# Performance work log

Measured on AMD Instinct MI355X. Metric: run time of the kernel, lower is better.

Reference implementation:

```python
import jax, jax.numpy as jnp
import numpy as np

N_NODES = 50000
N_EDGES = 800000
N_REL = 8
OUT_CH = 64      # latent dim of z
HID = 128        # hidden_channels
IN_CH = 128      # reconstructed feature dim
NEG_SLOPE = 0.2


def rgat_conv(x, src, dst, edge_type, weight, q, k, bias, num_nodes):
    """PyG RGATConv, heads=1, dim=1, additive-self-attention, across-relation.
    x: [N, in]; weight: [R, in, out]; q,k: [out, 1]; bias: [out]."""
    # per-relation transform of all nodes, then per-edge gather (same math as
    # per-edge bmm with weight[edge_type], avoids [E, in, out] intermediate)
    x_all = jnp.einsum('ni,rio->nro', x, weight)          # [N, R, out]
    x_j = x_all[src, edge_type]                            # [E, out]
    x_i = x_all[dst, edge_type]                            # [E, out]
    alpha = (x_i @ q + x_j @ k)[:, 0]                      # [E]
    alpha = jax.nn.leaky_relu(alpha, NEG_SLOPE)
    # scatter-softmax over destination neighborhoods
    m = jax.ops.segment_max(alpha, dst, num_segments=num_nodes)
    m = jnp.where(jnp.isfinite(m), m, 0.0)                 # empty segments -> 0
    ex = jnp.exp(alpha - m[dst])
    denom = jax.ops.segment_sum(ex, dst, num_segments=num_nodes)
    a = ex / (denom[dst] + 1e-16)                          # [E]
    out = jax.ops.segment_sum(a[:, None] * x_j, dst, num_segments=num_nodes)
    return out + bias


def setup_inputs() -> dict:
    key = jax.random.key(0)
    ks = jax.random.split(key, 12)
    z = jax.random.normal(ks[0], (N_NODES, OUT_CH), dtype=jnp.float32)
    edge_index = jax.random.randint(ks[1], (2, N_EDGES), 0, N_NODES, dtype=jnp.int32)
    edge_type = jax.random.randint(ks[2], (N_EDGES,), 0, N_REL, dtype=jnp.int32)

    def glorot(k_, shape):
        fan = shape[-2] + shape[-1]
        return jax.random.normal(k_, shape, dtype=jnp.float32) * jnp.sqrt(2.0 / fan)

    return {
        'z': z,
        'lin_w': glorot(ks[3], (HID, OUT_CH)),
        'lin_b': jnp.zeros((HID,), dtype=jnp.float32),
        'w1': glorot(ks[4], (N_REL, HID, HID)),
        'q1': glorot(ks[5], (HID, 1)),
        'k1': glorot(ks[6], (HID, 1)),
        'b1': jnp.zeros((HID,), dtype=jnp.float32),
        'w2': glorot(ks[7], (N_REL, HID, IN_CH)),
        'q2': glorot(ks[8], (IN_CH, 1)),
        'k2': glorot(ks[9], (IN_CH, 1)),
        'b2': jnp.zeros((IN_CH,), dtype=jnp.float32),
        'edge_index': edge_index,
        'edge_type': edge_type,
    }


def reference(z, lin_w, lin_b, w1, q1, k1, b1, w2, q2, k2, b2, edge_index, edge_type):
    num_nodes = z.shape[0]
    src, dst = edge_index[0], edge_index[1]
    h = z @ lin_w.T + lin_b                                 # nn.Linear
    h = jax.nn.relu(rgat_conv(h, src, dst, edge_type, w1, q1, k1, b1, num_nodes))
    # dropout is identity in eval mode
    recon_x = rgat_conv(h, src, dst, edge_type, w2, q2, k2, b2, num_nodes)
    return recon_x
```

## Files before the change

### kernel.cpp

```cpp
#include <hip/hip_runtime.h>
#include <hip/hip_bf16.h>
#include <cstdint>
#include <cstddef>

#define N_NODES 50000
#define N_EDGES 800000
#define NSEG    (N_NODES * 8)
#define HIST_BLKS 3125
#define WPREP_BLKS 1040
#define GLIN_BLKS 782
#define QK_BLKS 196

using frag_t = __attribute__((ext_vector_type(8))) short;
using f32x4  = __attribute__((ext_vector_type(4))) float;

typedef const __attribute__((address_space(1))) void* gptr_t;
typedef __attribute__((address_space(3))) void* lptr_t;

__device__ __forceinline__ short f2bf(float x) {
    __hip_bfloat16 h = __float2bfloat16(x);
    return *reinterpret_cast<short*>(&h);
}
__device__ __forceinline__ float bf2f(unsigned int u) {
    union { unsigned int i; float f; } v;
    v.i = u << 16;
    return v.f;
}
__device__ __forceinline__ float bf2f_hi(unsigned int u) {
    union { unsigned int i; float f; } v;
    v.i = u & 0xFFFF0000u;
    return v.f;
}
__device__ __forceinline__ unsigned int packbf2(float lo, float hi) {
    unsigned int a = (unsigned short)f2bf(lo);
    unsigned int b = (unsigned short)f2bf(hi);
    return a | (b << 16);
}


__global__ __launch_bounds__(256) void prep_mega(
        const int* __restrict__ dst, const int* __restrict__ et,
        int* __restrict__ deg8,
        const float* __restrict__ W1, const float* __restrict__ q1v,
        const float* __restrict__ k1v,
        const float* __restrict__ W2, const float* __restrict__ q2v,
        const float* __restrict__ k2v,
        short* __restrict__ Bf1, short* __restrict__ Bf2,
        float* __restrict__ wq1, float* __restrict__ wk1,
        float* __restrict__ wq2, float* __restrict__ wk2,
        const float* __restrict__ z, const float* __restrict__ lin_w,
        const float* __restrict__ lin_b,
        unsigned short* __restrict__ hb) {
    __shared__ float smem[32 * 64 + 32 * 128];
    int b = blockIdx.x, t = threadIdx.x;

    if (b < HIST_BLKS) {
        int e = b * 256 + t;
        if (e < N_EDGES) atomicAdd(&deg8[dst[e] * 8 + et[e]], 1);
        return;
    }
    b -= HIST_BLKS;

    if (b < WPREP_BLKS) {
        int g0 = b * 256 + t;
        int layer = (g0 >= 133120) ? 1 : 0;
        int g = g0 - layer * 133120;
        const float* W  = layer ? W2  : W1;
        const float* qv = layer ? q2v : q1v;
        const float* kv = layer ? k2v : k1v;
        short* Bf = layer ? Bf2 : Bf1;
        float* wq = layer ? wq2 : wq1;
        float* wk = layer ? wk2 : wk1;
        if (g < 131072) {
            int kk = g >> 7, o = g & 127;
            float v = W[(size_t)kk * 128 + o];
            Bf[(((size_t)(kk >> 3) * 128) + o) * 8 + (kk & 7)] = f2bf(v);
        } else {
            int h = g - 131072;
            if (h < 2048) {
                int which = h >> 10;
                int r = (h >> 7) & 7;
                int i = h & 127;
                const float* vec = which ? kv : qv;
                const float* wrow = W + ((size_t)r * 128 + i) * 128;
                float acc = 0.f;
                #pragma unroll 4
                for (int o = 0; o < 128; o++) acc = fmaf(wrow[o], vec[o], acc);
                (which ? wk : wq)[r * 128 + i] = acc;
            }
        }
        return;
    }
    b -= WPREP_BLKS;

    {
        float (*As)[64]  = (float (*)[64])smem;
        float (*Bs)[128] = (float (*)[128])(smem + 32 * 64);
        const int Kdim = 64;
        int n0 = b * 64;
        int rg = t >> 4, cg = t & 15;
        int an = t >> 2, ak = (t & 3) * 8;
        float acc[4][8] = {};

        for (int k0 = 0; k0 < Kdim; k0 += 32) {
            int gn = n0 + an;
            if (gn < N_NODES) {
                const float* ap = z + (size_t)gn * Kdim + k0 + ak;
                float4 v0 = *(const float4*)ap;
                float4 v1 = *(const float4*)(ap + 4);
                As[ak + 0][an] = v0.x; As[ak + 1][an] = v0.y;
                As[ak + 2][an] = v0.z; As[ak + 3][an] = v0.w;
                As[ak + 4][an] = v1.x; As[ak + 5][an] = v1.y;
                As[ak + 6][an] = v1.z; As[ak + 7][an] = v1.w;
            } else {
                #pragma unroll
                for (int c = 0; c < 8; c++) As[ak + c][an] = 0.f;
            }
            {
                int o = t >> 1, kh = (t & 1) * 16;
                const float* bp = lin_w + (size_t)o * Kdim + k0 + kh;
                #pragma unroll
                for (int j = 0; j < 4; j++) {
                    float4 v = ((const float4*)bp)[j];
                    Bs[kh + j * 4 + 0][o] = v.x;
                    Bs[kh + j * 4 + 1][o] = v.y;
                    Bs[kh + j * 4 + 2][o] = v.z;
                    Bs[kh + j * 4 + 3][o] = v.w;
                }
            }
            __syncthreads();
            #pragma unroll
            for (int k = 0; k < 32; k++) {
                float a[4], bb[8];
                *(float4*)&a[0] = *(const float4*)&As[k][rg * 4];
                *(float4*)&bb[0] = *(const float4*)&Bs[k][cg * 8];
                *(float4*)&bb[4] = *(const float4*)&Bs[k][cg * 8 + 4];
                #pragma unroll
                for (int i = 0; i < 4; i++)
                    #pragma unroll
                    for (int j = 0; j < 8; j++)
                        acc[i][j] = fmaf(a[i], bb[j], acc[i][j]);
            }
            __syncthreads();
        }
        #pragma unroll
        for (int i = 0; i < 4; i++) {
            int gn = n0 + rg * 4 + i;
            if (gn < N_NODES) {
                unsigned short us[8];
                #pragma unroll
                for (int j = 0; j < 8; j++)
                    us[j] = (unsigned short)f2bf(acc[i][j] + lin_b[cg * 8 + j]);
                *(int4*)(hb + (size_t)gn * 128 + cg * 8) = *(int4*)&us[0];
            }
        }
    }
}


__global__ __launch_bounds__(256) void scan_part(const int* __restrict__ deg8,
                                                 int* __restrict__ part, int M) {
    __shared__ int red[256];
    int t = threadIdx.x;
    int idx = blockIdx.x * 1024 + t * 4;
    int s = 0;
    if (idx + 3 < M) {
        int4 d = *(const int4*)(deg8 + idx);
        s = d.x + d.y + d.z + d.w;
    } else {
        for (int c = 0; c < 4; c++) if (idx + c < M) s += deg8[idx + c];
    }
    red[t] = s;
    __syncthreads();
    #pragma unroll
    for (int off = 128; off; off >>= 1) {
        if (t < off) red[t] += red[t + off];
        __syncthreads();
    }
    if (t == 0) part[blockIdx.x] = red[0];
}

__global__ __launch_bounds__(512) void scan_mid(int* __restrict__ part, int nparts,
                                                int* __restrict__ rowp, int M) {
    __shared__ int buf[512];
    int t = threadIdx.x;
    int own = (t < nparts) ? part[t] : 0;
    buf[t] = own;
    __syncthreads();
    for (int off = 1; off < 512; off <<= 1) {
        int v = buf[t];
        int u = (t >= off) ? buf[t - off] : 0;
        __syncthreads();
        buf[t] = v + u;
        __syncthreads();
    }
    if (t < nparts) part[t] = buf[t] - own;
    if (t == 511) rowp[M] = buf[511];
}

__global__ __launch_bounds__(256) void scan_fix(const int* __restrict__ deg8,
                                                const int* __restrict__ part,
                                                int* __restrict__ rowp,
                                                int* __restrict__ cursor, int M) {
    __shared__ int wsum[4];
    int t = threadIdx.x, lane = t & 63, w = t >> 6;
    int idx = blockIdx.x * 1024 + t * 4;
    int v0 = 0, v1 = 0, v2 = 0, v3 = 0;
    if (idx + 3 < M) {
        int4 d = *(const int4*)(deg8 + idx);
        v0 = d.x; v1 = d.y; v2 = d.z; v3 = d.w;
    } else {
        if (idx     < M) v0 = deg8[idx];
        if (idx + 1 < M) v1 = deg8[idx + 1];
        if (idx + 2 < M) v2 = deg8[idx + 2];
        if (idx + 3 < M) v3 = deg8[idx + 3];
    }
    int tsum = v0 + v1 + v2 + v3;
    int sc = tsum;
    #pragma unroll
    for (int off = 1; off < 64; off <<= 1) {
        int u = __shfl_up(sc, off, 64);
        if (lane >= off) sc += u;
    }
    if (lane == 63) wsum[w] = sc;
    __syncthreads();
    int woff = 0;
    for (int i = 0; i < w; i++) woff += wsum[i];
    int excl = part[blockIdx.x] + woff + sc - tsum;
    if (idx     < M) { rowp[idx]     = excl; cursor[idx]     = excl; } excl += v0;
    if (idx + 1 < M) { rowp[idx + 1] = excl; cursor[idx + 1] = excl; } excl += v1;
    if (idx + 2 < M) { rowp[idx + 2] = excl; cursor[idx + 2] = excl; } excl += v2;
    if (idx + 3 < M) { rowp[idx + 3] = excl; cursor[idx + 3] = excl; }
}


__global__ __launch_bounds__(256) void fill_qk(
        const int* __restrict__ src, const int* __restrict__ dst,
        const int* __restrict__ et, int* __restrict__ cursor,
        int* __restrict__ sorted,
        const unsigned short* __restrict__ xb,
        const float* __restrict__ wq, const float* __restrict__ wk,
        float* __restrict__ Q, float* __restrict__ K) {
    int b = blockIdx.x, t = threadIdx.x;

    if (b < HIST_BLKS) {
        int e = b * 256 + t;
        if (e < N_EDGES) {
            int pos = atomicAdd(&cursor[dst[e] * 8 + et[e]], 1);
            sorted[pos] = src[e] | (et[e] << 16);
        }
        return;
    }
    b -= HIST_BLKS;

    int n = b * 256 + t;
    if (n >= N_NODES) return;
    const uint2* row = (const uint2*)(xb + (size_t)n * 128);
    float aq[8] = {}, ak[8] = {};
    for (int i = 0; i < 32; i++) {
        uint2 d = row[i];
        float x0 = bf2f(d.x & 0xFFFFu);
        float x1 = bf2f(d.x >> 16);
        float x2 = bf2f(d.y & 0xFFFFu);
        float x3 = bf2f(d.y >> 16);
        int c = i * 4;
        #pragma unroll
        for (int r = 0; r < 8; r++) {
            const float* wqr = wq + r * 128 + c;
            const float* wkr = wk + r * 128 + c;
            aq[r] = fmaf(x0, wqr[0], fmaf(x1, wqr[1], fmaf(x2, wqr[2], fmaf(x3, wqr[3], aq[r]))));
            ak[r] = fmaf(x0, wkr[0], fmaf(x1, wkr[1], fmaf(x2, wkr[2], fmaf(x3, wkr[3], ak[r]))));
        }
    }
    float4* qp = (float4*)(Q + (size_t)n * 8);
    qp[0] = *(float4*)&aq[0];
    qp[1] = *(float4*)&aq[4];
    float4* kp = (float4*)(K + (size_t)n * 8);
    kp[0] = *(float4*)&ak[0];
    kp[1] = *(float4*)&ak[4];
}


__global__ __launch_bounds__(256) void qk_table_kernel(const unsigned short* __restrict__ xb,
                                                       const float* __restrict__ wq,
                                                       const float* __restrict__ wk,
                                                       float* __restrict__ Q,
                                                       float* __restrict__ K, int N) {
    int n = blockIdx.x * 256 + threadIdx.x;
    if (n >= N) return;
    const uint2* row = (const uint2*)(xb + (size_t)n * 128);
    float aq[8] = {}, ak[8] = {};
    for (int i = 0; i < 32; i++) {
        uint2 d = row[i];
        float x0 = bf2f(d.x & 0xFFFFu);
        float x1 = bf2f(d.x >> 16);
        float x2 = bf2f(d.y & 0xFFFFu);
        float x3 = bf2f(d.y >> 16);
        int c = i * 4;
        #pragma unroll
        for (int r = 0; r < 8; r++) {
            const float* wqr = wq + r * 128 + c;
            const float* wkr = wk + r * 128 + c;
            aq[r] = fmaf(x0, wqr[0], fmaf(x1, wqr[1], fmaf(x2, wqr[2], fmaf(x3, wqr[3], aq[r]))));
            ak[r] = fmaf(x0, wkr[0], fmaf(x1, wkr[1], fmaf(x2, wkr[2], fmaf(x3, wkr[3], ak[r]))));
        }
    }
    float4* qp = (float4*)(Q + (size_t)n * 8);
    qp[0] = *(float4*)&aq[0];
    qp[1] = *(float4*)&aq[4];
    float4* kp = (float4*)(K + (size_t)n * 8);
    kp[0] = *(float4*)&ak[0];
    kp[1] = *(float4*)&ak[4];
}


__global__ __launch_bounds__(512, 8) void fused_agg_gemm(
        const unsigned short* __restrict__ hb,
        const float* __restrict__ Q,
        const float* __restrict__ Kt,
        const int* __restrict__ rowp8,
        const int* __restrict__ sorted,
        const short* __restrict__ Bf,
        const float* __restrict__ bias,
        float* __restrict__ Cout,
        unsigned short* __restrict__ hbout,
        int N, int relu) {
    __shared__ short s_tile[16 * 1024];
    __shared__ uint2 stash[8][64];
    __shared__ int wcnt;
    unsigned int* sdw = (unsigned int*)s_tile;
    const char* hbB = (const char*)hb;

    int t = threadIdx.x;
    int w = t >> 6, lane = t & 63;
    int lhi = lane >> 4, llo = lane & 15;
    unsigned int lv4 = (unsigned int)lane * 4u;
    int n0 = blockIdx.x * 16;

    if (t == 0) wcnt = 0;
    __syncthreads();

    for (;;) {
        int row;
        if (lane == 0) row = atomicAdd(&wcnt, 1);
        row = __shfl(row, 0, 64);
        if (row >= 16) break;
        int n = n0 + row;
        float2 acc = {0.f, 0.f};
        int rcur = 0;
        auto flushw = [&](unsigned int val) {
            int kb = rcur * 16 + (lane >> 2);
            sdw[kb * 64 + ((row ^ (kb & 15)) * 4) + (lane & 3)] = val;
        };
        if (n >= N) {
            while (rcur < 8) { flushw(0u); rcur++; }
            continue;
        }
        int beg = rowp8[n * 8];
        int end = rowp8[n * 8 + 8];
        int deg = end - beg;
        if (deg == 0) {
            while (rcur < 8) { flushw(0u); rcur++; }
            continue;
        }

        if (deg <= 64) {
            int pk = 0;
            float a = -INFINITY;
            if (lane < deg) {
                pk = sorted[beg + lane];
                int srcn = pk & 0xFFFF, etj = pk >> 16;
                a = Q[(size_t)n * 8 + etj] + Kt[(size_t)srcn * 8 + etj];
                a = (a > 0.f) ? a : 0.2f * a;
            }
            float m = a;
            #pragma unroll
            for (int off = 32; off; off >>= 1) m = fmaxf(m, __shfl_xor(m, off, 64));
            float e = (lane < deg) ? __expf(a - m) : 0.f;
            float sum = e;
            #pragma unroll
            for (int off = 32; off; off >>= 1) sum += __shfl_xor(sum, off, 64);
            float wgt = e / (sum + 1e-16f);
            stash[w][lane] = make_uint2((unsigned int)(pk & 0xFFFF) << 8,
                                        (__float_as_uint(wgt) & ~7u) | (unsigned int)(pk >> 16));

            int j = 0;
            for (; j + 8 <= deg; j += 8) {
                uint2 ee[8]; unsigned int dd[8];
                #pragma unroll
                for (int i = 0; i < 8; i++) ee[i] = stash[w][j + i];
                #pragma unroll
                for (int i = 0; i < 8; i++)
                    dd[i] = *(const unsigned int*)(hbB + (ee[i].x | lv4));
                #pragma unroll
                for (int i = 0; i < 8; i++) {
                    int e0 = (int)(ee[i].y & 7u);
                    float w0 = __uint_as_float(ee[i].y);
                    while (rcur < e0) { flushw(packbf2(acc.x, acc.y)); acc.x = acc.y = 0.f; rcur++; }
                    acc.x = fmaf(w0, bf2f(dd[i]),    acc.x);
                    acc.y = fmaf(w0, bf2f_hi(dd[i]), acc.y);
                }
            }
            for (; j < deg; j++) {
                uint2 e1 = stash[w][j];
                unsigned int d0 = *(const unsigned int*)(hbB + (e1.x | lv4));
                int e0 = (int)(e1.y & 7u);
                float w0 = __uint_as_float(e1.y);
                while (rcur < e0) { flushw(packbf2(acc.x, acc.y)); acc.x = acc.y = 0.f; rcur++; }
                acc.x = fmaf(w0, bf2f(d0),    acc.x);
                acc.y = fmaf(w0, bf2f_hi(d0), acc.y);
            }
            while (rcur < 8) { flushw(packbf2(acc.x, acc.y)); acc.x = acc.y = 0.f; rcur++; }
        } else {
            auto logit = [&](int j) -> float {
                int pk2 = sorted[beg + j];
                int srcn = pk2 & 0xFFFF, etj = pk2 >> 16;
                float aa = Q[(size_t)n * 8 + etj] + Kt[(size_t)srcn * 8 + etj];
                return (aa > 0.f) ? aa : 0.2f * aa;
            };
            float m = -INFINITY;
            for (int j = lane; j < deg; j += 64) m = fmaxf(m, logit(j));
            #pragma unroll
            for (int off = 32; off; off >>= 1) m = fmaxf(m, __shfl_xor(m, off, 64));
            float sum = 0.f;
            for (int j = lane; j < deg; j += 64) sum += __expf(logit(j) - m);
            #pragma unroll
            for (int off = 32; off; off >>= 1) sum += __shfl_xor(sum, off, 64);
            float inv = 1.f / (sum + 1e-16f);

            for (int j0 = 0; j0 < deg; j0 += 64) {
                int cnt = min(64, deg - j0);
                if (lane < cnt) {
                    int pk = sorted[beg + j0 + lane];
                    int srcn = pk & 0xFFFF, etj = pk >> 16;
                    float aa = Q[(size_t)n * 8 + etj] + Kt[(size_t)srcn * 8 + etj];
                    aa = (aa > 0.f) ? aa : 0.2f * aa;
                    float wgt = __expf(aa - m) * inv;
                    stash[w][lane] = make_uint2((unsigned int)srcn << 8,
                                                (__float_as_uint(wgt) & ~7u) | (unsigned int)etj);
                }
                for (int j = 0; j < cnt; j++) {
                    uint2 e1 = stash[w][j];
                    unsigned int d0 = *(const unsigned int*)(hbB + (e1.x | lv4));
                    int e0 = (int)(e1.y & 7u);
                    float w0 = __uint_as_float(e1.y);
                    while (rcur < e0) { flushw(packbf2(acc.x, acc.y)); acc.x = acc.y = 0.f; rcur++; }
                    acc.x = fmaf(w0, bf2f(d0),    acc.x);
                    acc.y = fmaf(w0, bf2f_hi(d0), acc.y);
                }
            }
            while (rcur < 8) { flushw(packbf2(acc.x, acc.y)); acc.x = acc.y = 0.f; rcur++; }
        }
    }
    __syncthreads();

    int ctb = w;
    f32x4 acc0 = {};
    const char* BfB = (const char*)Bf;
    #pragma unroll 4
    for (int kq = 0; kq < 32; kq++) {
        int kb = kq * 4 + lhi;
        int d = kb * 64 + ((llo ^ (kb & 15)) * 4);
        frag_t a  = *(const frag_t*)(&sdw[d]);
        frag_t b0 = *(const frag_t*)(BfB + ((size_t)kb * 128 + ctb * 16 + llo) * 16);
        acc0 = __builtin_amdgcn_mfma_f32_16x16x32_bf16(a, b0, acc0, 0, 0, 0);
    }

    {
        int col = ctb * 16 + llo;
        float bv = bias[col];
        #pragma unroll
        for (int rg = 0; rg < 4; rg++) {
            int rown = n0 + lhi * 4 + rg;
            if (rown < N) {
                float v = acc0[rg] + bv;
                if (relu) v = fmaxf(v, 0.f);
                if (Cout)  Cout[(size_t)rown * 128 + col] = v;
                if (hbout) hbout[(size_t)rown * 128 + col] = (unsigned short)f2bf(v);
            }
        }
    }
}


extern "C" void kernel_launch(void* const* d_in, const int* in_sizes, int n_in,
                              void* d_out, int out_size, void* d_ws, size_t ws_size,
                              hipStream_t stream) {
    const float* z     = (const float*)d_in[0];
    const float* lin_w = (const float*)d_in[1];
    const float* lin_b = (const float*)d_in[2];
    const float* w1    = (const float*)d_in[3];
    const float* q1    = (const float*)d_in[4];
    const float* k1    = (const float*)d_in[5];
    const float* b1    = (const float*)d_in[6];
    const float* w2    = (const float*)d_in[7];
    const float* q2    = (const float*)d_in[8];
    const float* k2    = (const float*)d_in[9];
    const float* b2    = (const float*)d_in[10];
    const int*   ei    = (const int*)d_in[11];
    const int*   et    = (const int*)d_in[12];
    float* out = (float*)d_out;

    char* ws = (char*)d_ws;
    size_t off = 0;
    auto alloc = [&](size_t bytes) -> void* {
        void* p = ws + off;
        off += (bytes + 255) & ~(size_t)255;
        return p;
    };
    unsigned short* hb  = (unsigned short*)alloc((size_t)N_NODES * 128 * 2);
    unsigned short* hb2 = (unsigned short*)alloc((size_t)N_NODES * 128 * 2);
    float* Q     = (float*)alloc((size_t)N_NODES * 8 * 4);
    float* K     = (float*)alloc((size_t)N_NODES * 8 * 4);
    int* sorted  = (int*)alloc((size_t)N_EDGES * 4);
    int* deg8    = (int*)alloc((size_t)NSEG * 4);
    int* rowp8   = (int*)alloc((size_t)(NSEG + 1) * 4);
    int* cursor8 = (int*)alloc((size_t)NSEG * 4);
    int* part    = (int*)alloc(1024 * 4);
    float* wq1   = (float*)alloc(8 * 128 * 4);
    float* wk1   = (float*)alloc(8 * 128 * 4);
    float* wq2   = (float*)alloc(8 * 128 * 4);
    float* wk2   = (float*)alloc(8 * 128 * 4);
    short* Bf1   = (short*)alloc((size_t)1024 * 128 * 2);
    short* Bf2   = (short*)alloc((size_t)1024 * 128 * 2);

    const int* src = ei;
    const int* dst = ei + N_EDGES;

    const int M = NSEG;
    const int nparts = (M + 1023) / 1024;

    hipMemsetAsync(deg8, 0, (size_t)M * 4, stream);

    prep_mega<<<HIST_BLKS + WPREP_BLKS + GLIN_BLKS, 256, 0, stream>>>(
        dst, et, deg8,
        w1, q1, k1, w2, q2, k2, Bf1, Bf2, wq1, wk1, wq2, wk2,
        z, lin_w, lin_b, hb);

    scan_part<<<nparts, 256, 0, stream>>>(deg8, part, M);
    scan_mid<<<1, 512, 0, stream>>>(part, nparts, rowp8, M);
    scan_fix<<<nparts, 256, 0, stream>>>(deg8, part, rowp8, cursor8, M);

    fill_qk<<<HIST_BLKS + QK_BLKS, 256, 0, stream>>>(
        src, dst, et, cursor8, sorted, hb, wq1, wk1, Q, K);

    int fgrid = (N_NODES + 15) / 16;
    int qgrid = (N_NODES + 255) / 256;

    fused_agg_gemm<<<fgrid, 512, 0, stream>>>(hb, Q, K, rowp8, sorted, Bf1, b1,
                                              (float*)nullptr, hb2, N_NODES, 1);

    qk_table_kernel<<<qgrid, 256, 0, stream>>>(hb2, wq2, wk2, Q, K, N_NODES);

    fused_agg_gemm<<<fgrid, 512, 0, stream>>>(hb2, Q, K, rowp8, sorted, Bf2, b2,
                                              out, (unsigned short*)nullptr, N_NODES, 0);
}
```

Before: 349.0 us.

## Replace three-kernel scan with single-pass decoupled lookback scan

The three scan kernels (partial sums, mid scan, fixup) become a single kernel that uses a decoupled lookback over per-block descriptors held in global memory. This cuts two kernel launches and one pass over the degree array. The descriptors sit right after deg8, so the existing memset is extended to zero them. The lookback spins on atomics and assumes forward progress of earlier blocks; with 391 blocks all resident this should hold.

```diff
diff --git a/kernel.cpp b/kernel.cpp
--- a/kernel.cpp
+++ b/kernel.cpp
@@ -10,6 +10,7 @@
 #define WPREP_BLKS 1040
 #define GLIN_BLKS 782
 #define QK_BLKS 196
+#define NCHUNK 391
 
 using frag_t = __attribute__((ext_vector_type(8))) short;
 using f32x4  = __attribute__((ext_vector_type(4))) float;
@@ -158,53 +159,15 @@
 }
 
 
-__global__ __launch_bounds__(256) void scan_part(const int* __restrict__ deg8,
-                                                 int* __restrict__ part, int M) {
-    __shared__ int red[256];
-    int t = threadIdx.x;
-    int idx = blockIdx.x * 1024 + t * 4;
-    int s = 0;
-    if (idx + 3 < M) {
-        int4 d = *(const int4*)(deg8 + idx);
-        s = d.x + d.y + d.z + d.w;
-    } else {
-        for (int c = 0; c < 4; c++) if (idx + c < M) s += deg8[idx + c];
-    }
-    red[t] = s;
-    __syncthreads();
-    #pragma unroll
-    for (int off = 128; off; off >>= 1) {
-        if (t < off) red[t] += red[t + off];
-        __syncthreads();
-    }
-    if (t == 0) part[blockIdx.x] = red[0];
-}
-
-__global__ __launch_bounds__(512) void scan_mid(int* __restrict__ part, int nparts,
-                                                int* __restrict__ rowp, int M) {
-    __shared__ int buf[512];
-    int t = threadIdx.x;
-    int own = (t < nparts) ? part[t] : 0;
-    buf[t] = own;
-    __syncthreads();
-    for (int off = 1; off < 512; off <<= 1) {
-        int v = buf[t];
-        int u = (t >= off) ? buf[t - off] : 0;
-        __syncthreads();
-        buf[t] = v + u;
-        __syncthreads();
-    }
-    if (t < nparts) part[t] = buf[t] - own;
-    if (t == 511) rowp[M] = buf[511];
-}
-
-__global__ __launch_bounds__(256) void scan_fix(const int* __restrict__ deg8,
-                                                const int* __restrict__ part,
-                                                int* __restrict__ rowp,
-                                                int* __restrict__ cursor, int M) {
+__global__ __launch_bounds__(256) void scan_lookback(
+        const int* __restrict__ deg8,
+        unsigned long long* __restrict__ desc,
+        int* __restrict__ rowp, int* __restrict__ cursor, int M) {
     __shared__ int wsum[4];
-    int t = threadIdx.x, lane = t & 63, w = t >> 6;
-    int idx = blockIdx.x * 1024 + t * 4;
+    __shared__ int sbase;
+    int t = threadIdx.x, b = blockIdx.x;
+    int lane = t & 63, w = t >> 6;
+    int idx = b * 1024 + t * 4;
     int v0 = 0, v1 = 0, v2 = 0, v3 = 0;
     if (idx + 3 < M) {
         int4 d = *(const int4*)(deg8 + idx);
@@ -224,9 +187,28 @@
     }
     if (lane == 63) wsum[w] = sc;
     __syncthreads();
+
+    if (t == 0) {
+        unsigned int agg = (unsigned int)(wsum[0] + wsum[1] + wsum[2] + wsum[3]);
+        atomicExch(&desc[b], (1ULL << 32) | (unsigned long long)agg);
+        unsigned long long excl = 0;
+        int p = b - 1;
+        while (p >= 0) {
+            unsigned long long d = atomicAdd(&desc[p], 0ULL);
+            unsigned int f = (unsigned int)(d >> 32);
+            if (f == 2u) { excl += (unsigned int)d; break; }
+            if (f == 1u) { excl += (unsigned int)d; p--; continue; }
+            __builtin_amdgcn_s_sleep(1);
+        }
+        atomicExch(&desc[b], (2ULL << 32) | (excl + agg));
+        sbase = (int)excl;
+        if (b == NCHUNK - 1) rowp[M] = (int)(excl + agg);
+    }
+    __syncthreads();
+
     int woff = 0;
     for (int i = 0; i < w; i++) woff += wsum[i];
-    int excl = part[blockIdx.x] + woff + sc - tsum;
+    int excl = sbase + woff + sc - tsum;
     if (idx     < M) { rowp[idx]     = excl; cursor[idx]     = excl; } excl += v0;
     if (idx + 1 < M) { rowp[idx + 1] = excl; cursor[idx + 1] = excl; } excl += v1;
     if (idx + 2 < M) { rowp[idx + 2] = excl; cursor[idx + 2] = excl; } excl += v2;
@@ -514,9 +496,9 @@
     float* K     = (float*)alloc((size_t)N_NODES * 8 * 4);
     int* sorted  = (int*)alloc((size_t)N_EDGES * 4);
     int* deg8    = (int*)alloc((size_t)NSEG * 4);
+    unsigned long long* desc = (unsigned long long*)alloc(512 * 8);
     int* rowp8   = (int*)alloc((size_t)(NSEG + 1) * 4);
     int* cursor8 = (int*)alloc((size_t)NSEG * 4);
-    int* part    = (int*)alloc(1024 * 4);
     float* wq1   = (float*)alloc(8 * 128 * 4);
     float* wk1   = (float*)alloc(8 * 128 * 4);
     float* wq2   = (float*)alloc(8 * 128 * 4);
@@ -528,18 +510,15 @@
     const int* dst = ei + N_EDGES;
 
     const int M = NSEG;
-    const int nparts = (M + 1023) / 1024;
-
-    hipMemsetAsync(deg8, 0, (size_t)M * 4, stream);
+
+    hipMemsetAsync(deg8, 0, (size_t)M * 4 + 512 * 8, stream);
 
     prep_mega<<<HIST_BLKS + WPREP_BLKS + GLIN_BLKS, 256, 0, stream>>>(
         dst, et, deg8,
         w1, q1, k1, w2, q2, k2, Bf1, Bf2, wq1, wk1, wq2, wk2,
         z, lin_w, lin_b, hb);
 
-    scan_part<<<nparts, 256, 0, stream>>>(deg8, part, M);
-    scan_mid<<<1, 512, 0, stream>>>(part, nparts, rowp8, M);
-    scan_fix<<<nparts, 256, 0, stream>>>(deg8, part, rowp8, cursor8, M);
+    scan_lookback<<<NCHUNK, 256, 0, stream>>>(deg8, desc, rowp8, cursor8, M);
 
     fill_qk<<<HIST_BLKS + QK_BLKS, 256, 0, stream>>>(
         src, dst, et, cursor8, sorted, hb, wq1, wk1, Q, K);
```

Result: slower. 356.8 us (+2.2%).
